# Optimization experiments

Measured on AMD Instinct MI355X. Metric: run time of the kernel, lower is better.

The kernel has to match this reference:

```python
import jax, jax.numpy as jnp
import numpy as np

B, H, S, D = 2, 16, 2048, 128
SPARSITY = 0.1
NEG = -1.0e9


def local_mask(seq_len: int) -> jnp.ndarray:
    # window_size = max(1, int(seq_len * sparsity)); row i keeps cols [i-w//2, i+w//2]
    w = max(1, int(seq_len * SPARSITY))
    half = w // 2
    idx = jnp.arange(seq_len)
    diff = idx[None, :] - idx[:, None]  # j - i
    return ((diff >= -half) & (diff <= half)).astype(jnp.float32)


def setup_inputs() -> dict:
    key = jax.random.key(0)
    kq, kk, kv = jax.random.split(key, 3)
    return {
        "query": jax.random.normal(kq, (B, H, S, D), dtype=jnp.float32),
        "key": jax.random.normal(kk, (B, H, S, D), dtype=jnp.float32),
        "value": jax.random.normal(kv, (B, H, S, D), dtype=jnp.float32),
    }


def reference(query, key, value):
    head_dim = query.shape[-1]
    seq_len_k = key.shape[2]
    m = local_mask(seq_len_k)[None, None]  # [1,1,S,S]
    scores = jnp.einsum("bhqd,bhkd->bhqk", query, key) / jnp.sqrt(
        jnp.asarray(head_dim, query.dtype)
    )
    scores = scores * m + (1.0 - m) * NEG
    probs = jax.nn.softmax(scores, axis=-1)
    context = jnp.einsum("bhqk,bhkd->bhqd", probs, value)
    return context, probs
```

## Files before the change

### kernel.cpp

```cpp
#include <hip/hip_runtime.h>
#include <math.h>


namespace {
constexpr int Sc = 2048, Dc = 128;
constexpr int HALFW = 102;
constexpr float SCALE = 0.08838834764831845f;
constexpr int TQ  = 32;
constexpr int CT  = 256;
constexpr int KST = 136;
constexpr int PST = 260;
}

typedef __bf16 bf16x8 __attribute__((ext_vector_type(8)));
typedef float  f32x16 __attribute__((ext_vector_type(16)));

__device__ __forceinline__ unsigned short f2bf(float f) {
    unsigned u = __float_as_uint(f);
    u += 0x7fffu + ((u >> 16) & 1u);
    return (unsigned short)(u >> 16);
}

__global__ __launch_bounds__(256, 2) void sparse_attn_mfma(
    const float* __restrict__ Q, const float* __restrict__ K,
    const float* __restrict__ V, float* __restrict__ ctx,
    float* __restrict__ probs)
{
    __shared__ __align__(16) unsigned short Qs[TQ * KST];
    __shared__ __align__(16) unsigned char  Kbuf[128 * KST * 2];
    __shared__ float Ps[TQ * PST];
    __shared__ float red[TQ][4];
    __shared__ float rowM[TQ];
    __shared__ float rowSinv[TQ];

    const int tid  = threadIdx.x;
    const int lane = tid & 63;
    const int w    = tid >> 6;
    const int lo   = lane & 31;
    const int hi   = lane >> 5;

    const int wid = (blockIdx.x & 7) * 256 + (blockIdx.x >> 3);
    const int bh  = wid >> 6;
    const int qt  = wid & 63;
    const int i0  = qt * TQ;
    const int js0 = max(0, i0 - HALFW);
    const int jend = min(js0 + CT, Sc);

    const size_t rowbase = (size_t)bh * Sc;
    float* probsBase = probs + (rowbase + i0) * (size_t)Sc;

    {
        const int headN = js0 & 3;
        const int tailN = (4 - (jend & 3)) & 3;
        const int hn = headN + tailN;
        if (hn == 4) {
            int r = tid >> 2, s = tid & 3;
            if (r < TQ) {
                int col = (s < headN) ? (js0 - headN + s) : (jend + s - headN);
                probsBase[(size_t)r * Sc + col] = 0.0f;
            }
        } else if (hn == 2) {
            int r = tid >> 1, s = tid & 1;
            if (r < TQ) {
                int col = (s < headN) ? (js0 - headN + s) : (jend + s - headN);
                probsBase[(size_t)r * Sc + col] = 0.0f;
            }
        }
        const int leftQ   = (js0 - headN) >> 2;
        const int rightQ0 = (jend + tailN) >> 2;
        const float4 z4 = make_float4(0.f, 0.f, 0.f, 0.f);
        for (int r = 0; r < TQ; ++r) {
            float4* p4 = (float4*)(probsBase + (size_t)r * Sc);
            for (int c = tid; c < leftQ; c += 256) p4[c] = z4;
            for (int c = rightQ0 + tid; c < Sc / 4; c += 256) p4[c] = z4;
        }
    }

    {
        const float4* Q4 = (const float4*)(Q + (rowbase + i0) * Dc);
        #pragma unroll
        for (int it = 0; it < 4; ++it) {
            int idx = tid + 256 * it;
            int r = idx >> 5, d4 = idx & 31;
            float4 q4 = Q4[r * 32 + d4];
            ushort4 b;
            b.x = f2bf(q4.x); b.y = f2bf(q4.y); b.z = f2bf(q4.z); b.w = f2bf(q4.w);
            *(ushort4*)&Qs[r * KST + d4 * 4] = b;
        }
    }

    unsigned short* Ks = (unsigned short*)Kbuf;
    const float4* K4 = (const float4*)(K + rowbase * Dc);
    const float4* V4 = (const float4*)(V + rowbase * Dc);

    f32x16 accE[2];
    #pragma unroll
    for (int ch = 0; ch < 2; ++ch) {
        #pragma unroll
        for (int it = 0; it < 16; ++it) {
            int idx = tid + 256 * it;
            int r = idx >> 5, d4 = idx & 31;
            int jn = js0 + ch * 128 + r;
            if (jn > Sc - 1) jn = Sc - 1;
            float4 k4 = K4[(size_t)jn * 32 + d4];
            ushort4 b;
            b.x = f2bf(k4.x); b.y = f2bf(k4.y); b.z = f2bf(k4.z); b.w = f2bf(k4.w);
            *(ushort4*)&Ks[r * KST + d4 * 4] = b;
        }
        __syncthreads();
        f32x16 acc;
        #pragma unroll
        for (int i = 0; i < 16; ++i) acc[i] = 0.0f;
        const unsigned short* qrow = &Qs[lo * KST + hi * 8];
        const unsigned short* krow = &Ks[(w * 32 + lo) * KST + hi * 8];
        #pragma unroll
        for (int dk = 0; dk < 8; ++dk) {
            bf16x8 a = *(const bf16x8*)(qrow + dk * 16);
            bf16x8 b = *(const bf16x8*)(krow + dk * 16);
            acc = __builtin_amdgcn_mfma_f32_32x32x16_bf16(a, b, acc, 0, 0, 0);
        }
        accE[ch] = acc;
        __syncthreads();
    }

    const int cg0 = js0 + w * 32 + lo;
    {
        float mred[16];
        #pragma unroll
        for (int i = 0; i < 16; ++i) {
            int rl = (i & 3) + 8 * (i >> 2) + 4 * hi;
            int rg = i0 + rl;
            float m = -3.0e38f;
            #pragma unroll
            for (int ch = 0; ch < 2; ++ch) {
                int cg = cg0 + ch * 128;
                bool valid = (cg < Sc) & (cg >= rg - HALFW) & (cg <= rg + HALFW);
                float sv = valid ? accE[ch][i] * SCALE : -3.0e38f;
                accE[ch][i] = sv;
                m = fmaxf(m, sv);
            }
            mred[i] = m;
        }
        #pragma unroll
        for (int mk = 1; mk < 32; mk <<= 1) {
            #pragma unroll
            for (int i = 0; i < 16; ++i)
                mred[i] = fmaxf(mred[i], __shfl_xor(mred[i], mk, 64));
        }
        if (lo == 0) {
            #pragma unroll
            for (int i = 0; i < 16; ++i) {
                int rl = (i & 3) + 8 * (i >> 2) + 4 * hi;
                red[rl][w] = mred[i];
            }
        }
    }
    __syncthreads();
    if (tid < 128) {
        int rr = tid >> 2, sl = tid & 3;
        float v = red[rr][sl];
        v = fmaxf(v, __shfl_xor(v, 1, 64));
        v = fmaxf(v, __shfl_xor(v, 2, 64));
        if (sl == 0) rowM[rr] = v;
    }
    __syncthreads();

    {
        float sred[16];
        #pragma unroll
        for (int i = 0; i < 16; ++i) {
            int rl = (i & 3) + 8 * (i >> 2) + 4 * hi;
            float rm = rowM[rl];
            float e0 = __expf(accE[0][i] - rm);
            float e1 = __expf(accE[1][i] - rm);
            accE[0][i] = e0; accE[1][i] = e1;
            sred[i] = e0 + e1;
        }
        #pragma unroll
        for (int mk = 1; mk < 32; mk <<= 1) {
            #pragma unroll
            for (int i = 0; i < 16; ++i)
                sred[i] += __shfl_xor(sred[i], mk, 64);
        }
        if (lo == 0) {
            #pragma unroll
            for (int i = 0; i < 16; ++i) {
                int rl = (i & 3) + 8 * (i >> 2) + 4 * hi;
                red[rl][w] = sred[i];
            }
        }
    }
    __syncthreads();
    if (tid < 128) {
        int rr = tid >> 2, sl = tid & 3;
        float v = red[rr][sl];
        v += __shfl_xor(v, 1, 64);
        v += __shfl_xor(v, 2, 64);
        if (sl == 0) rowSinv[rr] = 1.0f / v;
    }
    __syncthreads();

    #pragma unroll
    for (int i = 0; i < 16; ++i) {
        int rl = (i & 3) + 8 * (i >> 2) + 4 * hi;
        float inv = rowSinv[rl];
        float* prow = probsBase + (size_t)rl * Sc;
        #pragma unroll
        for (int ch = 0; ch < 2; ++ch) {
            int cg = cg0 + ch * 128;
            float p = accE[ch][i] * inv;
            Ps[rl * PST + (cg - js0)] = p;
            if (cg < Sc) prow[cg] = p;
        }
    }
    __syncthreads();

    float4* Vsf = (float4*)Kbuf;
    const int pr = tid >> 3;
    const int dg = tid & 7;
    float4 o0 = make_float4(0.f,0.f,0.f,0.f), o1 = o0, o2 = o0, o3 = o0;
    #pragma unroll
    for (int ch4 = 0; ch4 < 4; ++ch4) {
        #pragma unroll
        for (int it = 0; it < 8; ++it) {
            int idx = tid + 256 * it;
            int r = idx >> 5, d4 = idx & 31;
            int jn = js0 + ch4 * 64 + r;
            if (jn > Sc - 1) jn = Sc - 1;
            Vsf[r * 32 + d4] = V4[(size_t)jn * 32 + d4];
        }
        __syncthreads();
        const float* prow = &Ps[pr * PST + ch4 * 64];
        #pragma unroll 2
        for (int k = 0; k < 64; ++k) {
            float p = prow[k];
            const float4* vr = &Vsf[k * 32 + dg * 4];
            float4 v0 = vr[0], v1 = vr[1], v2 = vr[2], v3 = vr[3];
            o0.x = fmaf(p, v0.x, o0.x); o0.y = fmaf(p, v0.y, o0.y);
            o0.z = fmaf(p, v0.z, o0.z); o0.w = fmaf(p, v0.w, o0.w);
            o1.x = fmaf(p, v1.x, o1.x); o1.y = fmaf(p, v1.y, o1.y);
            o1.z = fmaf(p, v1.z, o1.z); o1.w = fmaf(p, v1.w, o1.w);
            o2.x = fmaf(p, v2.x, o2.x); o2.y = fmaf(p, v2.y, o2.y);
            o2.z = fmaf(p, v2.z, o2.z); o2.w = fmaf(p, v2.w, o2.w);
            o3.x = fmaf(p, v3.x, o3.x); o3.y = fmaf(p, v3.y, o3.y);
            o3.z = fmaf(p, v3.z, o3.z); o3.w = fmaf(p, v3.w, o3.w);
        }
        __syncthreads();
    }
    float4* C4 = (float4*)ctx + (rowbase + i0 + pr) * 32 + dg * 4;
    C4[0] = o0; C4[1] = o1; C4[2] = o2; C4[3] = o3;
}

extern "C" void kernel_launch(void* const* d_in, const int* in_sizes, int n_in,
                              void* d_out, int out_size, void* d_ws, size_t ws_size,
                              hipStream_t stream) {
    const float* Q = (const float*)d_in[0];
    const float* K = (const float*)d_in[1];
    const float* V = (const float*)d_in[2];
    float* out   = (float*)d_out;
    float* ctx   = out;
    float* probs = out + (size_t)2 * 16 * 2048 * 128;

    dim3 grid(2 * 16 * (Sc / TQ));
    dim3 block(256);
    sparse_attn_mfma<<<grid, block, 0, stream>>>(Q, K, V, ctx, probs);
}
```

Baseline: 748.3 us.

## Use nontemporal stores, unify LDS, and restructure PV loop with register tiling

Probability and context writes become nontemporal stores, so the large write-only probs output does not pollute cache. LDS is merged into one aliased buffer with P stored transposed, and V is held in a padded layout. The P·V stage is reorganized so each lane computes a 4-row by 16-column tile over a quarter of the k range, then reduces across lanes with shuffles. This raises arithmetic intensity per LDS load, in exchange for the extra shuffle reductions and higher register pressure.

```diff
diff --git a/kernel.cpp b/kernel.cpp
--- a/kernel.cpp
+++ b/kernel.cpp
@@ -9,11 +9,18 @@
 constexpr int TQ  = 32;
 constexpr int CT  = 256;
 constexpr int KST = 136;
-constexpr int PST = 260;
+constexpr int VST = 132;
+constexpr int PTS = 36;
+constexpr int OFF_KBUF = 0;
+constexpr int OFF_PST  = 34816;
+constexpr int OFF_QS   = 34816;
+constexpr int OFF_RED  = 34816 + 36864;
+constexpr int LDS_TOTAL = OFF_RED + 512 + 128 + 128;
 }
 
 typedef __bf16 bf16x8 __attribute__((ext_vector_type(8)));
 typedef float  f32x16 __attribute__((ext_vector_type(16)));
+typedef float  fx4    __attribute__((ext_vector_type(4)));
 
 __device__ __forceinline__ unsigned short f2bf(float f) {
     unsigned u = __float_as_uint(f);
@@ -26,12 +33,14 @@
     const float* __restrict__ V, float* __restrict__ ctx,
     float* __restrict__ probs)
 {
-    __shared__ __align__(16) unsigned short Qs[TQ * KST];
-    __shared__ __align__(16) unsigned char  Kbuf[128 * KST * 2];
-    __shared__ float Ps[TQ * PST];
-    __shared__ float red[TQ][4];
-    __shared__ float rowM[TQ];
-    __shared__ float rowSinv[TQ];
+    __shared__ __align__(16) unsigned char smem[LDS_TOTAL];
+    unsigned short* Ks   = (unsigned short*)(smem + OFF_KBUF);
+    float*          Vsf  = (float*)(smem + OFF_KBUF);
+    float*          Ps_t = (float*)(smem + OFF_PST);
+    unsigned short* Qs   = (unsigned short*)(smem + OFF_QS);
+    float (*red)[4]      = (float(*)[4])(smem + OFF_RED);
+    float* rowM          = (float*)(smem + OFF_RED + 512);
+    float* rowSinv       = (float*)(smem + OFF_RED + 512 + 128);
 
     const int tid  = threadIdx.x;
     const int lane = tid & 63;
@@ -57,22 +66,24 @@
             int r = tid >> 2, s = tid & 3;
             if (r < TQ) {
                 int col = (s < headN) ? (js0 - headN + s) : (jend + s - headN);
-                probsBase[(size_t)r * Sc + col] = 0.0f;
+                __builtin_nontemporal_store(0.0f, probsBase + (size_t)r * Sc + col);
             }
         } else if (hn == 2) {
             int r = tid >> 1, s = tid & 1;
             if (r < TQ) {
                 int col = (s < headN) ? (js0 - headN + s) : (jend + s - headN);
-                probsBase[(size_t)r * Sc + col] = 0.0f;
+                __builtin_nontemporal_store(0.0f, probsBase + (size_t)r * Sc + col);
             }
         }
         const int leftQ   = (js0 - headN) >> 2;
         const int rightQ0 = (jend + tailN) >> 2;
-        const float4 z4 = make_float4(0.f, 0.f, 0.f, 0.f);
+        const fx4 z4 = {0.f, 0.f, 0.f, 0.f};
         for (int r = 0; r < TQ; ++r) {
-            float4* p4 = (float4*)(probsBase + (size_t)r * Sc);
-            for (int c = tid; c < leftQ; c += 256) p4[c] = z4;
-            for (int c = rightQ0 + tid; c < Sc / 4; c += 256) p4[c] = z4;
+            fx4* p4 = (fx4*)(probsBase + (size_t)r * Sc);
+            for (int c = tid; c < leftQ; c += 256)
+                __builtin_nontemporal_store(z4, p4 + c);
+            for (int c = rightQ0 + tid; c < Sc / 4; c += 256)
+                __builtin_nontemporal_store(z4, p4 + c);
         }
     }
 
@@ -89,7 +100,6 @@
         }
     }
 
-    unsigned short* Ks = (unsigned short*)Kbuf;
     const float4* K4 = (const float4*)(K + rowbase * Dc);
     const float4* V4 = (const float4*)(V + rowbase * Dc);
 
@@ -209,16 +219,21 @@
         for (int ch = 0; ch < 2; ++ch) {
             int cg = cg0 + ch * 128;
             float p = accE[ch][i] * inv;
-            Ps[rl * PST + (cg - js0)] = p;
-            if (cg < Sc) prow[cg] = p;
-        }
-    }
-    __syncthreads();
-
-    float4* Vsf = (float4*)Kbuf;
-    const int pr = tid >> 3;
-    const int dg = tid & 7;
-    float4 o0 = make_float4(0.f,0.f,0.f,0.f), o1 = o0, o2 = o0, o3 = o0;
+            Ps_t[(cg - js0) * PTS + rl] = p;
+            if (cg < Sc) __builtin_nontemporal_store(p, prow + cg);
+        }
+    }
+    __syncthreads();
+
+    const int kp  = lane & 3;
+    const int dgq = (lane >> 2) & 1;
+    const int rg  = lane >> 3;
+    fx4 o[4][4];
+    #pragma unroll
+    for (int c = 0; c < 4; ++c)
+        #pragma unroll
+        for (int j = 0; j < 4; ++j) o[c][j] = (fx4){0.f, 0.f, 0.f, 0.f};
+
     #pragma unroll
     for (int ch4 = 0; ch4 < 4; ++ch4) {
         #pragma unroll
@@ -227,28 +242,58 @@
             int r = idx >> 5, d4 = idx & 31;
             int jn = js0 + ch4 * 64 + r;
             if (jn > Sc - 1) jn = Sc - 1;
-            Vsf[r * 32 + d4] = V4[(size_t)jn * 32 + d4];
+            float4 v4g = V4[(size_t)jn * 32 + d4];
+            *(float4*)&Vsf[r * VST + d4 * 4] = v4g;
         }
         __syncthreads();
-        const float* prow = &Ps[pr * PST + ch4 * 64];
-        #pragma unroll 2
-        for (int k = 0; k < 64; ++k) {
-            float p = prow[k];
-            const float4* vr = &Vsf[k * 32 + dg * 4];
-            float4 v0 = vr[0], v1 = vr[1], v2 = vr[2], v3 = vr[3];
-            o0.x = fmaf(p, v0.x, o0.x); o0.y = fmaf(p, v0.y, o0.y);
-            o0.z = fmaf(p, v0.z, o0.z); o0.w = fmaf(p, v0.w, o0.w);
-            o1.x = fmaf(p, v1.x, o1.x); o1.y = fmaf(p, v1.y, o1.y);
-            o1.z = fmaf(p, v1.z, o1.z); o1.w = fmaf(p, v1.w, o1.w);
-            o2.x = fmaf(p, v2.x, o2.x); o2.y = fmaf(p, v2.y, o2.y);
-            o2.z = fmaf(p, v2.z, o2.z); o2.w = fmaf(p, v2.w, o2.w);
-            o3.x = fmaf(p, v3.x, o3.x); o3.y = fmaf(p, v3.y, o3.y);
-            o3.z = fmaf(p, v3.z, o3.z); o3.w = fmaf(p, v3.w, o3.w);
+        const float* Pbase = &Ps_t[(ch4 * 64) * PTS + 4 * rg];
+        const float* Vbase = &Vsf[w * 32 + dgq * 16];
+        #pragma unroll 4
+        for (int kk = 0; kk < 16; ++kk) {
+            int k = 4 * kk + kp;
+            fx4 p4 = *(const fx4*)(Pbase + k * PTS);
+            const float* vr = Vbase + k * VST;
+            fx4 v0 = *(const fx4*)(vr);
+            fx4 v1 = *(const fx4*)(vr + 4);
+            fx4 v2 = *(const fx4*)(vr + 8);
+            fx4 v3 = *(const fx4*)(vr + 12);
+            #pragma unroll
+            for (int c = 0; c < 4; ++c) {
+                float pc = p4[c];
+                o[c][0] += v0 * pc;
+                o[c][1] += v1 * pc;
+                o[c][2] += v2 * pc;
+                o[c][3] += v3 * pc;
+            }
         }
         __syncthreads();
     }
-    float4* C4 = (float4*)ctx + (rowbase + i0 + pr) * 32 + dg * 4;
-    C4[0] = o0; C4[1] = o1; C4[2] = o2; C4[3] = o3;
+
+    #pragma unroll
+    for (int c = 0; c < 4; ++c) {
+        #pragma unroll
+        for (int j = 0; j < 4; ++j) {
+            fx4 t = o[c][j];
+            #pragma unroll
+            for (int comp = 0; comp < 4; ++comp) {
+                float s = t[comp];
+                s += __shfl_xor(s, 1, 64);
+                s += __shfl_xor(s, 2, 64);
+                t[comp] = s;
+            }
+            o[c][j] = t;
+        }
+    }
+    if (kp == 0) {
+        #pragma unroll
+        for (int c = 0; c < 4; ++c) {
+            float* crow = ctx + (rowbase + i0 + 4 * rg + c) * (size_t)Dc
+                        + w * 32 + dgq * 16;
+            #pragma unroll
+            for (int j = 0; j < 4; ++j)
+                __builtin_nontemporal_store(o[c][j], (fx4*)crow + j);
+        }
+    }
 }
 
 extern "C" void kernel_launch(void* const* d_in, const int* in_sizes, int n_in,
```

After: 692.9 us. 1.08x faster.
